# Kernel tuning notes

Hardware: AMD Instinct MI355X
Metric: run time of the kernel (lower is better)

The kernel has to match this reference:

```python
import jax, jax.numpy as jnp
import numpy as np

POINT_DIM = 3  # chunk size along feature axis (module default point_dim)
M_KINF = 1.0   # default buffer torch.ones(1)


def setup_inputs() -> dict:
    key = jax.random.key(0)
    vct = jax.random.normal(key, (2048, 48), dtype=jnp.float32)  # (N, D), K = D/POINT_DIM = 16
    # learned parameter [tau, lambda] exactly as in __init__ with M_Kinf = 1
    tau = (1.0 / M_KINF) * 0.99
    lam = float(np.sqrt(1.0 - tau * tau * M_KINF * M_KINF) * 0.99)
    posnum = jnp.array([tau, lam], dtype=jnp.float32)
    return {"vct": vct, "posnum": posnum}


def _chunk_dists(vct):
    """Pairwise Euclidean distances per feature chunk: (K, N, N).
    Equivalent to torch.linalg.norm(vct_h_chunk - vct_chunk[..., None], dim=-2),
    computed via gram matrices with a safe sqrt (grad 0 at zero distance,
    matching torch's norm subgradient)."""
    N, D = vct.shape
    K = D // POINT_DIM
    ch = vct.reshape(N, K, POINT_DIM)
    sq = jnp.sum(ch * ch, axis=-1)                   # (N, K)
    gram = jnp.einsum('nkd,mkd->knm', ch, ch)        # (K, N, N)
    sqk = sq.T                                       # (K, N)
    d2 = jnp.maximum(sqk[:, :, None] + sqk[:, None, :] - 2.0 * gram, 0.0)
    safe = jnp.where(d2 > 0, d2, 1.0)
    return jnp.sqrt(safe) * (d2 > 0).astype(vct.dtype)


def reference(vct, posnum):
    dist = _chunk_dists(vct)                          # (K, N, N)
    inner_prod = M_KINF - dist                        # stack of (M_Kinf - norm)
    inner_res = 1.0 / (1.0 - posnum[0] ** 2 * inner_prod)
    cp = jnp.cumprod(inner_res, axis=0)               # fused prefix product over K
    K = cp.shape[0]
    # weights lambda^{2k} for k = 1..K (loop in original = weighted cumprod sum)
    weights = posnum[1] ** (2.0 * jnp.arange(1, K + 1, dtype=vct.dtype))
    kernel_matrix = 1.0 + jnp.einsum('k,knm->nm', weights, cp)
    return kernel_matrix
```

## Files before the change

### kernel.cpp

```cpp
#include <hip/hip_runtime.h>
#include <math.h>

#define N 2048
#define D 48
#define K 16
#define TILE 32
#define NT (N / TILE)
#define NBLK (NT * (NT + 1) / 2)


__global__ __launch_bounds__(128, 5)
void volt_tri(const float* __restrict__ vct, const float* __restrict__ posnum,
              float* __restrict__ out) {
#pragma clang fp contract(off)
    __shared__ float4 AB[2][K * TILE];
    float* T = reinterpret_cast<float*>(AB);

    const int tid = threadIdx.x;

    int t = blockIdx.x;
    int by = 0;
    while ((by + 1) * NT - ((by + 1) * by) / 2 <= t) ++by;
    const int bx = by + (t - (by * NT - (by * (by - 1)) / 2));

    const int row0 = by * TILE, col0 = bx * TILE;

    const float tau = posnum[0];
    const float lam = posnum[1];
    const float t2 = tau * tau;
    const float l2 = lam * lam;

    for (int it = 0; it < 8; ++it) {
        int task = tid + 128 * it;
        int set = task >> 9;
        int rk = task & 511;
        int r = rk & 31, k = rk >> 5;
        int base = ((set ? col0 : row0) + r) * D + k * 3;
        float x0 = vct[base + 0];
        float x1 = vct[base + 1];
        float x2 = vct[base + 2];
        float q0 = x0 * x0, q1 = x1 * x1, q2 = x2 * x2;
        asm volatile("" : "+v"(q0), "+v"(q1), "+v"(q2));
        float s02 = q0 + q2;
        asm volatile("" : "+v"(s02));
        float s = s02 + q1;
        AB[set][k * TILE + r] = make_float4(x0, x1, x2, s);
    }
    __syncthreads();

    const int tx = tid & 15;
    const int ty = tid >> 4;

    float G[4][2], Pd[4][2];
#pragma unroll
    for (int i = 0; i < 4; ++i)
#pragma unroll
        for (int j = 0; j < 2; ++j) { G[i][j] = 0.0f; Pd[i][j] = 1.0f; }

#pragma unroll
    for (int k = K - 1; k >= 0; --k) {
        float4 a[4], b[2];
#pragma unroll
        for (int i = 0; i < 4; ++i) a[i] = AB[0][k * TILE + ty + 8 * i];
#pragma unroll
        for (int j = 0; j < 2; ++j) b[j] = AB[1][k * TILE + tx + 16 * j];
#pragma unroll
        for (int i = 0; i < 4; ++i)
#pragma unroll
            for (int j = 0; j < 2; ++j) {
                float g = __builtin_fmaf(a[i].z, b[j].z,
                          __builtin_fmaf(a[i].y, b[j].y, a[i].x * b[j].x));
                float t1 = a[i].w + b[j].w;
                float d2 = __builtin_fmaf(-2.0f, g, t1);
                float dist = __builtin_amdgcn_sqrtf(fmaxf(d2, 0.0f));
                float ip  = 1.0f - dist;
                float den = 1.0f - t2 * ip;
                G[i][j]  = l2 * (Pd[i][j] + G[i][j]);
                Pd[i][j] = Pd[i][j] * den;
            }
    }

    float val[4][2];
#pragma unroll
    for (int i = 0; i < 4; ++i)
#pragma unroll
        for (int j = 0; j < 2; ++j)
            val[i][j] = 1.0f + G[i][j] * __builtin_amdgcn_rcpf(Pd[i][j]);

#pragma unroll
    for (int i = 0; i < 4; ++i) {
        int r = ty + 8 * i;
#pragma unroll
        for (int j = 0; j < 2; ++j)
            out[(size_t)(row0 + r) * N + (col0 + tx + 16 * j)] = val[i][j];
    }

    if (bx != by) {
        __syncthreads();
#pragma unroll
        for (int i = 0; i < 4; ++i)
#pragma unroll
            for (int j = 0; j < 2; ++j)
                T[(tx + 16 * j) * 33 + (ty + 8 * i)] = val[i][j];
        __syncthreads();
#pragma unroll
        for (int i = 0; i < 4; ++i) {
            int rr = ty + 8 * i;
#pragma unroll
            for (int j = 0; j < 2; ++j) {
                int cc = tx + 16 * j;
                out[(size_t)(col0 + rr) * N + (row0 + cc)] = T[rr * 33 + cc];
            }
        }
    }
}

extern "C" void kernel_launch(void* const* d_in, const int* in_sizes, int n_in,
                              void* d_out, int out_size, void* d_ws, size_t ws_size,
                              hipStream_t stream) {
    const float* vct    = (const float*)d_in[0];
    const float* posnum = (const float*)d_in[1];
    float* out          = (float*)d_out;

    volt_tri<<<NBLK, 128, 0, stream>>>(vct, posnum, out);
}
```

Measured before the change: 25.40 us.

## Vectorize tile loads with float4, fold denominator into one FMA, relax occupancy bound

The tile load now has each thread fetch 12 contiguous floats as three float4 loads covering four 3-wide chunks, replacing eight strided scalar-triple loads. The per-element denominator 1 - t2*(1 - dist) is rewritten as fma(t2, dist, 1 - t2), saving an instruction in the inner loop. The launch-bounds minimum-blocks hint drops from 5 to 4, giving the compiler more registers per thread. The algebraic rewrite changes rounding slightly, and the lower occupancy hint may reduce latency hiding.

```diff
diff --git a/kernel.cpp b/kernel.cpp
--- a/kernel.cpp
+++ b/kernel.cpp
@@ -9,7 +9,7 @@
 #define NBLK (NT * (NT + 1) / 2)
 
 
-__global__ __launch_bounds__(128, 5)
+__global__ __launch_bounds__(128, 4)
 void volt_tri(const float* __restrict__ vct, const float* __restrict__ posnum,
               float* __restrict__ out) {
 #pragma clang fp contract(off)
@@ -22,29 +22,38 @@
     int by = 0;
     while ((by + 1) * NT - ((by + 1) * by) / 2 <= t) ++by;
     const int bx = by + (t - (by * NT - (by * (by - 1)) / 2));
-
     const int row0 = by * TILE, col0 = bx * TILE;
 
     const float tau = posnum[0];
     const float lam = posnum[1];
     const float t2 = tau * tau;
     const float l2 = lam * lam;
+    const float c0 = 1.0f - t2;
 
-    for (int it = 0; it < 8; ++it) {
-        int task = tid + 128 * it;
-        int set = task >> 9;
-        int rk = task & 511;
-        int r = rk & 31, k = rk >> 5;
-        int base = ((set ? col0 : row0) + r) * D + k * 3;
-        float x0 = vct[base + 0];
-        float x1 = vct[base + 1];
-        float x2 = vct[base + 2];
-        float q0 = x0 * x0, q1 = x1 * x1, q2 = x2 * x2;
-        asm volatile("" : "+v"(q0), "+v"(q1), "+v"(q2));
-        float s02 = q0 + q2;
-        asm volatile("" : "+v"(s02));
-        float s = s02 + q1;
-        AB[set][k * TILE + r] = make_float4(x0, x1, x2, s);
+    const int r = tid >> 2;
+    const int q = tid & 3;
+#pragma unroll
+    for (int set = 0; set < 2; ++set) {
+        const float* rowp = &vct[((set ? col0 : row0) + r) * D + q * 12];
+        const float4 v0 = *reinterpret_cast<const float4*>(rowp);
+        const float4 v1 = *reinterpret_cast<const float4*>(rowp + 4);
+        const float4 v2 = *reinterpret_cast<const float4*>(rowp + 8);
+        float cx[4][3] = {
+            {v0.x, v0.y, v0.z},
+            {v0.w, v1.x, v1.y},
+            {v1.z, v1.w, v2.x},
+            {v2.y, v2.z, v2.w},
+        };
+#pragma unroll
+        for (int c = 0; c < 4; ++c) {
+            float x0 = cx[c][0], x1 = cx[c][1], x2 = cx[c][2];
+            float q0 = x0 * x0, q1 = x1 * x1, q2 = x2 * x2;
+            asm volatile("" : "+v"(q0), "+v"(q1), "+v"(q2));
+            float s02 = q0 + q2;
+            asm volatile("" : "+v"(s02));
+            float s = s02 + q1;
+            AB[set][(4 * q + c) * TILE + r] = make_float4(x0, x1, x2, s);
+        }
     }
     __syncthreads();
 
@@ -73,8 +82,7 @@
                 float t1 = a[i].w + b[j].w;
                 float d2 = __builtin_fmaf(-2.0f, g, t1);
                 float dist = __builtin_amdgcn_sqrtf(fmaxf(d2, 0.0f));
-                float ip  = 1.0f - dist;
-                float den = 1.0f - t2 * ip;
+                float den = __builtin_fmaf(t2, dist, c0);
                 G[i][j]  = l2 * (Pd[i][j] + G[i][j]);
                 Pd[i][j] = Pd[i][j] * den;
             }
@@ -89,10 +97,10 @@
 
 #pragma unroll
     for (int i = 0; i < 4; ++i) {
-        int r = ty + 8 * i;
+        int rr = ty + 8 * i;
 #pragma unroll
         for (int j = 0; j < 2; ++j)
-            out[(size_t)(row0 + r) * N + (col0 + tx + 16 * j)] = val[i][j];
+            out[(size_t)(row0 + rr) * N + (col0 + tx + 16 * j)] = val[i][j];
     }
 
     if (bx != by) {
```

After: 23.85 us. 1.06x faster.
